# Performance work log

Measured on AMD Instinct MI355X. Metric: run time of the kernel, lower is better.

## Reference

```python
import jax, jax.numpy as jnp
import numpy as np

M, N, D = 100000, 64, 128  # points, channels, voxel grid side


def setup_inputs() -> dict:
    key = jax.random.key(0)
    k1, k2, k3, k4, k5 = jax.random.split(key, 5)
    rng = np.random.default_rng(0)
    # unique occupied voxels in a D^3 grid (Minkowski coords are unique)
    lin = rng.choice(D ** 3, size=M, replace=False)
    coords = np.stack(np.unravel_index(lin, (D, D, D)), axis=1).astype(np.int32)
    w_scale = 0.02  # ~1/sqrt(fan_in=27*N)
    return {
        "feats": jax.random.normal(k1, (M, N), dtype=jnp.float32),
        "W1": jax.random.normal(k2, (27, N, N), dtype=jnp.float32) * w_scale,
        "b1": jax.random.normal(k3, (N,), dtype=jnp.float32) * 0.01,
        "W2": jax.random.normal(k4, (27, N, N), dtype=jnp.float32) * w_scale,
        "b2": jax.random.normal(k5, (N,), dtype=jnp.float32) * 0.01,
        "coords": jnp.asarray(coords),
        "grid_size": D,
    }


def reference(feats, W1, b1, W2, b2, coords, grid_size):
    Dg = grid_size
    m = feats.shape[0]
    # dense hash: linear voxel id -> point index (-1 if empty)
    lin = (coords[:, 0].astype(jnp.int32) * Dg + coords[:, 1]) * Dg + coords[:, 2]
    lookup = jnp.full((Dg * Dg * Dg,), -1, dtype=jnp.int32).at[lin].set(
        jnp.arange(m, dtype=jnp.int32))
    offsets = jnp.array([[i, j, k] for i in (-1, 0, 1) for j in (-1, 0, 1)
                         for k in (-1, 0, 1)], dtype=jnp.int32)  # [27,3]

    def sparse_conv(x, W, b):
        # out[u] = b + sum_k W_k^T gather(x, u+off_k); scan over 27 offsets keeps
        # only one [M,N] gathered buffer live (memory-bound gather-GEMM-scatter)
        def step(acc, wk_off):
            W_k, off = wk_off
            nc = coords + off  # [M,3]
            inb = jnp.all((nc >= 0) & (nc < Dg), axis=1)
            nlin = (nc[:, 0] * Dg + nc[:, 1]) * Dg + nc[:, 2]
            nidx = lookup[jnp.where(inb, nlin, 0)]
            valid = inb & (nidx >= 0)
            g = jnp.where(valid[:, None], x[jnp.maximum(nidx, 0)], 0.0)  # [M,N]
            return acc + g @ W_k, None
        init = jnp.zeros_like(x) + b
        out, _ = jax.lax.scan(step, init, (W, offsets))
        return out

    h = jax.nn.relu(sparse_conv(feats, W1, b1))
    return jax.nn.relu(sparse_conv(h, W2, b2))
```

## Files before the change

kernel.cpp:

```cpp
#include <hip/hip_runtime.h>
#include <hip/hip_bf16.h>
#include <cstdint>
#include <cstddef>

typedef _Float16 half8 __attribute__((ext_vector_type(8)));
typedef float floatx16 __attribute__((ext_vector_type(16)));

#define DGRID 128
#define D3 (DGRID * DGRID * DGRID)
#define WSZ (2 * 27 * 4096)

__global__ void prep(const int* __restrict__ coords, const float* __restrict__ feats,
                     const float* __restrict__ W1, const float* __restrict__ W2,
                     int* __restrict__ lookup, _Float16* __restrict__ Whf,
                     _Float16* __restrict__ h0, _Float16* __restrict__ h, int M) {
    int tid = blockIdx.x * 256 + threadIdx.x;
    if (tid < WSZ) {
        int idx = tid;
        int j = idx & 7;
        int l = (idx >> 3) & 63;
        int f = (idx >> 9) & 7;
        int kL = idx >> 12;
        int k = kL % 27, L = kL / 27;
        int kk = f & 3, ct = f >> 2;
        int c = kk * 16 + (l >> 5) * 8 + j;
        int n = ct * 32 + (l & 31);
        const float* W = L ? W2 : W1;
        Whf[idx] = (_Float16)W[k * 4096 + c * 64 + n];
        return;
    }
    tid -= WSZ;
    if (tid < M) {
        int x = coords[3 * tid], y = coords[3 * tid + 1], z = coords[3 * tid + 2];
        lookup[(x * DGRID + y) * DGRID + z] = tid;
        return;
    }
    tid -= M;
    if (tid < 64) {
        h0[(size_t)M * 64 + tid] = (_Float16)0.f;
        h[(size_t)M * 64 + tid] = (_Float16)0.f;
        return;
    }
    tid -= 64;
    if (tid < M * 8) {
        const float4* src = (const float4*)feats + (size_t)tid * 2;
        float4 f0 = src[0], f1 = src[1];
        half8 v;
        v[0] = (_Float16)f0.x; v[1] = (_Float16)f0.y;
        v[2] = (_Float16)f0.z; v[3] = (_Float16)f0.w;
        v[4] = (_Float16)f1.x; v[5] = (_Float16)f1.y;
        v[6] = (_Float16)f1.z; v[7] = (_Float16)f1.w;
        ((half8*)h0)[tid] = v;
    }
}

__global__ void build_nbr(const int* __restrict__ coords, const int* __restrict__ lookup,
                          int* __restrict__ nbr, int M) {
    int m = blockIdx.x * 256 + threadIdx.x;
    if (m >= M) return;
    int x = coords[3 * m], y = coords[3 * m + 1], z = coords[3 * m + 2];
#pragma unroll
    for (int k = 0; k < 27; ++k) {
        int nx = x + k / 9 - 1, ny = y + (k / 3) % 3 - 1, nz = z + k % 3 - 1;
        int nidx = M;
        if (((unsigned)nx < DGRID) && ((unsigned)ny < DGRID) && ((unsigned)nz < DGRID)) {
            int v = lookup[(nx * DGRID + ny) * DGRID + nz];
            if ((unsigned)v < (unsigned)M) nidx = v;
        }
        nbr[(size_t)k * M + m] = nidx;
    }
}

template <bool OUT_F16>
__global__ __launch_bounds__(64, 2) void spconv(const _Float16* __restrict__ x,
                                                const _Float16* __restrict__ Whf,
                                                const float* __restrict__ bias,
                                                const int* __restrict__ nbr,
                                                void* __restrict__ outp, int M) {
    const int lane = threadIdx.x;
    const int lrow = lane & 31;
    const int lhalf = lane >> 5;
    const int mw = blockIdx.x * 64;
    const int gm0 = mw + lrow;
    const int gm1 = mw + 32 + lrow;
    const int gmc0 = gm0 < M ? gm0 : M - 1;
    const int gmc1 = gm1 < M ? gm1 : M - 1;

    floatx16 acc[4];
#pragma unroll
    for (int i = 0; i < 4; ++i)
#pragma unroll
        for (int j = 0; j < 16; ++j) acc[i][j] = 0.0f;

    const half8* wb = (const half8*)Whf + lane;

    auto loadB = [&](half8* dst, int k) {
#pragma unroll
        for (int f = 0; f < 8; ++f) dst[f] = wb[(k * 8 + f) * 64];
    };
    auto loadA = [&](half8* dst, int n0, int n1) {
        const half8* p0 = (const half8*)(x + (size_t)n0 * 64 + lhalf * 8);
        const half8* p1 = (const half8*)(x + (size_t)n1 * 64 + lhalf * 8);
#pragma unroll
        for (int kk = 0; kk < 4; ++kk) {
            dst[kk] = p0[kk * 2];
            dst[4 + kk] = p1[kk * 2];
        }
    };

    int nv0[4], nv1[4];
#pragma unroll
    for (int j = 0; j < 3; ++j) {
        nv0[j] = nbr[(size_t)j * M + gmc0];
        nv1[j] = nbr[(size_t)j * M + gmc1];
    }

    half8 Ar[3][8], Br[2][8];
    loadB(Br[0], 0);
    loadA(Ar[0], nv0[0], nv1[0]);
    loadA(Ar[1], nv0[1], nv1[1]);

#pragma unroll
    for (int i = 0; i < 27; ++i) {
        {
            int jn = i + 3;
            if (jn < 27) {
                nv0[jn & 3] = nbr[(size_t)jn * M + gmc0];
                nv1[jn & 3] = nbr[(size_t)jn * M + gmc1];
            }
        }
        if (i + 1 < 27) loadB(Br[(i + 1) & 1], i + 1);
        {
            int ja = i + 2;
            if (ja < 27) loadA(Ar[ja % 3], nv0[ja & 3], nv1[ja & 3]);
        }
        __builtin_amdgcn_sched_barrier(0);
        half8* A = Ar[i % 3];
        half8* B = Br[i & 1];
#pragma unroll
        for (int kk = 0; kk < 4; ++kk)
#pragma unroll
            for (int rt = 0; rt < 2; ++rt)
#pragma unroll
                for (int ct = 0; ct < 2; ++ct)
                    acc[rt * 2 + ct] = __builtin_amdgcn_mfma_f32_32x32x16_f16(
                        A[rt * 4 + kk], B[ct * 4 + kk], acc[rt * 2 + ct], 0, 0, 0);
    }

    const float bv0 = bias[lrow], bv1 = bias[32 + lrow];
#pragma unroll
    for (int rt = 0; rt < 2; ++rt)
#pragma unroll
        for (int ct = 0; ct < 2; ++ct) {
            const float bb = ct ? bv1 : bv0;
#pragma unroll
            for (int reg = 0; reg < 16; ++reg) {
                int row = (reg & 3) + 8 * (reg >> 2) + 4 * lhalf;
                int g = mw + rt * 32 + row;
                if (g < M) {
                    float v = acc[rt * 2 + ct][reg] + bb;
                    v = v > 0.f ? v : 0.f;
                    size_t off = (size_t)g * 64 + ct * 32 + lrow;
                    if constexpr (OUT_F16)
                        ((_Float16*)outp)[off] = (_Float16)v;
                    else
                        ((float*)outp)[off] = v;
                }
            }
        }
}

extern "C" void kernel_launch(void* const* d_in, const int* in_sizes, int n_in,
                              void* d_out, int out_size, void* d_ws, size_t ws_size,
                              hipStream_t stream) {
    const float* feats = (const float*)d_in[0];
    const float* W1 = (const float*)d_in[1];
    const float* b1 = (const float*)d_in[2];
    const float* W2 = (const float*)d_in[3];
    const float* b2 = (const float*)d_in[4];
    const int* coords = (const int*)d_in[5];
    const int M = in_sizes[0] / 64;

    int* lookup = (int*)d_ws;
    int* nbr = lookup + (size_t)D3;
    _Float16* h = (_Float16*)(nbr + (size_t)27 * M);
    _Float16* h0 = h + (size_t)(M + 1) * 64;
    _Float16* Whf = h0 + (size_t)(M + 1) * 64;
    size_t need = (size_t)D3 * 4 + (size_t)27 * M * 4 +
                  2 * (size_t)(M + 1) * 64 * 2 + (size_t)WSZ * 2;
    if (ws_size < need) return;

    long long pt = (long long)WSZ + M + 64 + (long long)M * 8;
    prep<<<(int)((pt + 255) / 256), 256, 0, stream>>>(coords, feats, W1, W2, lookup, Whf,
                                                      h0, h, M);
    build_nbr<<<(M + 255) / 256, 256, 0, stream>>>(coords, lookup, nbr, M);

    int cb = (M + 63) / 64;
    spconv<true><<<cb, 64, 0, stream>>>(h0, Whf, b1, nbr, (void*)h, M);
    spconv<false><<<cb, 64, 0, stream>>>(h, Whf + (size_t)27 * 4096, b2, nbr, d_out, M);
}
```

Before: 186.6 us.

## Fuse prep, neighbor build and both convolutions into one cooperative kernel

Replaces the four separate launches with a single cooperative persistent kernel that uses grid-wide syncs between prep, neighbor-table build and the two conv layers. Work is distributed with grid-stride loops, and each 256-thread block runs four waves, each looping over 64-row tiles. This removes launch gaps but caps the grid at 512 blocks and binds the conv to persistent scheduling with launch bounds of 256 threads. That can cut occupancy or latency hiding compared with one small block per tile. A fallback multi-kernel path remains if the cooperative launch fails.

```diff
diff --git a/kernel.cpp b/kernel.cpp
--- a/kernel.cpp
+++ b/kernel.cpp
@@ -1,7 +1,10 @@
 #include <hip/hip_runtime.h>
 #include <hip/hip_bf16.h>
+#include <hip/hip_cooperative_groups.h>
 #include <cstdint>
 #include <cstddef>
+
+namespace cg = cooperative_groups;
 
 typedef _Float16 half8 __attribute__((ext_vector_type(8)));
 typedef float floatx16 __attribute__((ext_vector_type(16)));
@@ -10,13 +13,15 @@
 #define D3 (DGRID * DGRID * DGRID)
 #define WSZ (2 * 27 * 4096)
 
-__global__ void prep(const int* __restrict__ coords, const float* __restrict__ feats,
-                     const float* __restrict__ W1, const float* __restrict__ W2,
-                     int* __restrict__ lookup, _Float16* __restrict__ Whf,
-                     _Float16* __restrict__ h0, _Float16* __restrict__ h, int M) {
-    int tid = blockIdx.x * 256 + threadIdx.x;
-    if (tid < WSZ) {
-        int idx = tid;
+__device__ __forceinline__ void do_prep(int tid, int NT, const int* __restrict__ coords,
+                                        const float* __restrict__ feats,
+                                        const float* __restrict__ W1,
+                                        const float* __restrict__ W2,
+                                        int* __restrict__ lookup,
+                                        _Float16* __restrict__ Whf,
+                                        _Float16* __restrict__ h0,
+                                        _Float16* __restrict__ h, int M) {
+    for (int idx = tid; idx < WSZ; idx += NT) {
         int j = idx & 7;
         int l = (idx >> 3) & 63;
         int f = (idx >> 9) & 7;
@@ -27,60 +32,55 @@
         int n = ct * 32 + (l & 31);
         const float* W = L ? W2 : W1;
         Whf[idx] = (_Float16)W[k * 4096 + c * 64 + n];
-        return;
-    }
-    tid -= WSZ;
-    if (tid < M) {
-        int x = coords[3 * tid], y = coords[3 * tid + 1], z = coords[3 * tid + 2];
-        lookup[(x * DGRID + y) * DGRID + z] = tid;
-        return;
-    }
-    tid -= M;
-    if (tid < 64) {
-        h0[(size_t)M * 64 + tid] = (_Float16)0.f;
-        h[(size_t)M * 64 + tid] = (_Float16)0.f;
-        return;
-    }
-    tid -= 64;
-    if (tid < M * 8) {
-        const float4* src = (const float4*)feats + (size_t)tid * 2;
+    }
+    for (int i = tid; i < M * 8; i += NT) {
+        const float4* src = (const float4*)feats + (size_t)i * 2;
         float4 f0 = src[0], f1 = src[1];
         half8 v;
         v[0] = (_Float16)f0.x; v[1] = (_Float16)f0.y;
         v[2] = (_Float16)f0.z; v[3] = (_Float16)f0.w;
         v[4] = (_Float16)f1.x; v[5] = (_Float16)f1.y;
         v[6] = (_Float16)f1.z; v[7] = (_Float16)f1.w;
-        ((half8*)h0)[tid] = v;
-    }
-}
-
-__global__ void build_nbr(const int* __restrict__ coords, const int* __restrict__ lookup,
-                          int* __restrict__ nbr, int M) {
-    int m = blockIdx.x * 256 + threadIdx.x;
-    if (m >= M) return;
-    int x = coords[3 * m], y = coords[3 * m + 1], z = coords[3 * m + 2];
-#pragma unroll
-    for (int k = 0; k < 27; ++k) {
-        int nx = x + k / 9 - 1, ny = y + (k / 3) % 3 - 1, nz = z + k % 3 - 1;
-        int nidx = M;
-        if (((unsigned)nx < DGRID) && ((unsigned)ny < DGRID) && ((unsigned)nz < DGRID)) {
-            int v = lookup[(nx * DGRID + ny) * DGRID + nz];
-            if ((unsigned)v < (unsigned)M) nidx = v;
-        }
-        nbr[(size_t)k * M + m] = nidx;
+        ((half8*)h0)[i] = v;
+    }
+    for (int m = tid; m < M; m += NT) {
+        int x = coords[3 * m], y = coords[3 * m + 1], z = coords[3 * m + 2];
+        lookup[(x * DGRID + y) * DGRID + z] = m;
+    }
+    if (tid < 64) {
+        h0[(size_t)M * 64 + tid] = (_Float16)0.f;
+        h[(size_t)M * 64 + tid] = (_Float16)0.f;
+    }
+}
+
+__device__ __forceinline__ void do_nbr(int tid, int NT, const int* __restrict__ coords,
+                                       const int* __restrict__ lookup,
+                                       int* __restrict__ nbr, int M) {
+    for (int m = tid; m < M; m += NT) {
+        int x = coords[3 * m], y = coords[3 * m + 1], z = coords[3 * m + 2];
+#pragma unroll
+        for (int k = 0; k < 27; ++k) {
+            int nx = x + k / 9 - 1, ny = y + (k / 3) % 3 - 1, nz = z + k % 3 - 1;
+            int nidx = M;
+            if (((unsigned)nx < DGRID) && ((unsigned)ny < DGRID) &&
+                ((unsigned)nz < DGRID)) {
+                int v = lookup[(nx * DGRID + ny) * DGRID + nz];
+                if ((unsigned)v < (unsigned)M) nidx = v;
+            }
+            nbr[(size_t)k * M + m] = nidx;
+        }
     }
 }
 
 template <bool OUT_F16>
-__global__ __launch_bounds__(64, 2) void spconv(const _Float16* __restrict__ x,
-                                                const _Float16* __restrict__ Whf,
-                                                const float* __restrict__ bias,
-                                                const int* __restrict__ nbr,
-                                                void* __restrict__ outp, int M) {
-    const int lane = threadIdx.x;
+__device__ __forceinline__ void conv_tile(const _Float16* __restrict__ x,
+                                          const _Float16* __restrict__ Wfrag,
+                                          const float* __restrict__ bias,
+                                          const int* __restrict__ nbr,
+                                          void* __restrict__ outp, int M, int lane,
+                                          int mw) {
     const int lrow = lane & 31;
     const int lhalf = lane >> 5;
-    const int mw = blockIdx.x * 64;
     const int gm0 = mw + lrow;
     const int gm1 = mw + 32 + lrow;
     const int gmc0 = gm0 < M ? gm0 : M - 1;
@@ -92,7 +92,7 @@
 #pragma unroll
         for (int j = 0; j < 16; ++j) acc[i][j] = 0.0f;
 
-    const half8* wb = (const half8*)Whf + lane;
+    const half8* wb = (const half8*)Wfrag + lane;
 
     auto loadB = [&](half8* dst, int k) {
 #pragma unroll
@@ -170,6 +170,59 @@
         }
 }
 
+__global__ __launch_bounds__(256, 2) void fused(const int* __restrict__ coords,
+                                                const float* __restrict__ feats,
+                                                const float* __restrict__ W1,
+                                                const float* __restrict__ b1,
+                                                const float* __restrict__ W2,
+                                                const float* __restrict__ b2,
+                                                int* __restrict__ lookup,
+                                                _Float16* __restrict__ Whf,
+                                                _Float16* __restrict__ h0,
+                                                _Float16* __restrict__ h,
+                                                int* __restrict__ nbr,
+                                                float* __restrict__ out, int M) {
+    cg::grid_group grid = cg::this_grid();
+    const int tid = blockIdx.x * 256 + threadIdx.x;
+    const int NT = gridDim.x * 256;
+
+    do_prep(tid, NT, coords, feats, W1, W2, lookup, Whf, h0, h, M);
+    grid.sync();
+    do_nbr(tid, NT, coords, lookup, nbr, M);
+    grid.sync();
+
+    const int lane = threadIdx.x & 63;
+    const int wave = blockIdx.x * 4 + (threadIdx.x >> 6);
+    const int NW = gridDim.x * 4;
+    const int NTILES = (M + 63) / 64;
+
+    for (int t = wave; t < NTILES; t += NW)
+        conv_tile<true>(h0, Whf, b1, nbr, (void*)h, M, lane, t * 64);
+    grid.sync();
+    for (int t = wave; t < NTILES; t += NW)
+        conv_tile<false>(h, Whf + (size_t)27 * 4096, b2, nbr, (void*)out, M, lane, t * 64);
+}
+
+__global__ __launch_bounds__(256) void prep_k(const int* coords, const float* feats,
+                                              const float* W1, const float* W2,
+                                              int* lookup, _Float16* Whf, _Float16* h0,
+                                              _Float16* h, int M) {
+    do_prep(blockIdx.x * 256 + threadIdx.x, gridDim.x * 256, coords, feats, W1, W2,
+            lookup, Whf, h0, h, M);
+}
+__global__ __launch_bounds__(256) void nbr_k(const int* coords, const int* lookup,
+                                             int* nbr, int M) {
+    do_nbr(blockIdx.x * 256 + threadIdx.x, gridDim.x * 256, coords, lookup, nbr, M);
+}
+template <bool OUT_F16>
+__global__ __launch_bounds__(64, 2) void conv_k(const _Float16* __restrict__ x,
+                                                const _Float16* __restrict__ Whf,
+                                                const float* __restrict__ bias,
+                                                const int* __restrict__ nbr,
+                                                void* __restrict__ outp, int M) {
+    conv_tile<OUT_F16>(x, Whf, bias, nbr, outp, M, (int)threadIdx.x, blockIdx.x * 64);
+}
+
 extern "C" void kernel_launch(void* const* d_in, const int* in_sizes, int n_in,
                               void* d_out, int out_size, void* d_ws, size_t ws_size,
                               hipStream_t stream) {
@@ -190,12 +243,25 @@
                   2 * (size_t)(M + 1) * 64 * 2 + (size_t)WSZ * 2;
     if (ws_size < need) return;
 
-    long long pt = (long long)WSZ + M + 64 + (long long)M * 8;
-    prep<<<(int)((pt + 255) / 256), 256, 0, stream>>>(coords, feats, W1, W2, lookup, Whf,
-                                                      h0, h, M);
-    build_nbr<<<(M + 255) / 256, 256, 0, stream>>>(coords, lookup, nbr, M);
-
-    int cb = (M + 63) / 64;
-    spconv<true><<<cb, 64, 0, stream>>>(h0, Whf, b1, nbr, (void*)h, M);
-    spconv<false><<<cb, 64, 0, stream>>>(h, Whf + (size_t)27 * 4096, b2, nbr, d_out, M);
-}
+    const int NTILES = (M + 63) / 64;
+    int coopGrid = (NTILES + 3) / 4;
+    if (coopGrid > 512) coopGrid = 512;
+    float* out = (float*)d_out;
+
+    int Mv = M;
+    void* args[] = {(void*)&coords, (void*)&feats, (void*)&W1,  (void*)&b1,
+                    (void*)&W2,     (void*)&b2,    (void*)&lookup, (void*)&Whf,
+                    (void*)&h0,     (void*)&h,     (void*)&nbr,  (void*)&out,
+                    (void*)&Mv};
+    hipError_t e = hipLaunchCooperativeKernel((const void*)fused, dim3(coopGrid),
+                                              dim3(256), args, 0, stream);
+    if (e != hipSuccess) {
+        long long pw = (long long)WSZ + (long long)M * 8;
+        prep_k<<<(int)((pw + 255) / 256), 256, 0, stream>>>(coords, feats, W1, W2, lookup,
+                                                            Whf, h0, h, M);
+        nbr_k<<<(M + 255) / 256, 256, 0, stream>>>(coords, lookup, nbr, M);
+        conv_k<true><<<NTILES, 64, 0, stream>>>(h0, Whf, b1, nbr, (void*)h, M);
+        conv_k<false><<<NTILES, 64, 0, stream>>>(h, Whf + (size_t)27 * 4096, b2, nbr,
+                                                 d_out, M);
+    }
+}
```

Result: slower. 515.9 us (+176.5%).

## Halve spconv rows per wave and batch z-neighbor lookups in build_nbr

Applied to the files above, without the earlier changes.

The sparse conv kernel now processes 32 output rows per 64-lane block instead of 64, which halves accumulator and A-register usage and doubles the block count. The occupancy hint is raised from 2 to 3. Separately, build_nbr loads three consecutive z entries of the lookup table in one 12-byte read per (dx,dy) pair instead of 27 scalar loads. The trade-off is that each weight tile is now reused over fewer rows, so weight reads from cache double per output row.

```diff
diff --git a/kernel.cpp b/kernel.cpp
--- a/kernel.cpp
+++ b/kernel.cpp
@@ -9,6 +9,8 @@
 #define DGRID 128
 #define D3 (DGRID * DGRID * DGRID)
 #define WSZ (2 * 27 * 4096)
+
+struct __attribute__((aligned(4))) I3 { int a, b, c; };
 
 __global__ void prep(const int* __restrict__ coords, const float* __restrict__ feats,
                      const float* __restrict__ W1, const float* __restrict__ W2,
@@ -59,20 +61,35 @@
     int m = blockIdx.x * 256 + threadIdx.x;
     if (m >= M) return;
     int x = coords[3 * m], y = coords[3 * m + 1], z = coords[3 * m + 2];
-#pragma unroll
-    for (int k = 0; k < 27; ++k) {
-        int nx = x + k / 9 - 1, ny = y + (k / 3) % 3 - 1, nz = z + k % 3 - 1;
-        int nidx = M;
-        if (((unsigned)nx < DGRID) && ((unsigned)ny < DGRID) && ((unsigned)nz < DGRID)) {
-            int v = lookup[(nx * DGRID + ny) * DGRID + nz];
-            if ((unsigned)v < (unsigned)M) nidx = v;
-        }
-        nbr[(size_t)k * M + m] = nidx;
+    int zlo = z - 1;
+    if (zlo < 0) zlo = 0;
+    if (zlo > DGRID - 3) zlo = DGRID - 3;
+    const int zi = z - zlo;
+#pragma unroll
+    for (int dx = -1; dx <= 1; ++dx) {
+#pragma unroll
+        for (int dy = -1; dy <= 1; ++dy) {
+            int nx = x + dx, ny = y + dy;
+            int v0 = -1, v1 = -1, v2 = -1;
+            if (((unsigned)nx < DGRID) && ((unsigned)ny < DGRID)) {
+                I3 t = *(const I3*)(lookup + ((nx * DGRID + ny) * DGRID + zlo));
+                v0 = t.a; v1 = t.b; v2 = t.c;
+            }
+#pragma unroll
+            for (int dz = -1; dz <= 1; ++dz) {
+                int zc = z + dz;
+                int i = zi + dz;
+                int val = (i == 0) ? v0 : (i == 1) ? v1 : v2;
+                int nidx = M;
+                if (((unsigned)zc < DGRID) && ((unsigned)val < (unsigned)M)) nidx = val;
+                nbr[(size_t)((dx + 1) * 9 + (dy + 1) * 3 + (dz + 1)) * M + m] = nidx;
+            }
+        }
     }
 }
 
 template <bool OUT_F16>
-__global__ __launch_bounds__(64, 2) void spconv(const _Float16* __restrict__ x,
+__global__ __launch_bounds__(64, 3) void spconv(const _Float16* __restrict__ x,
                                                 const _Float16* __restrict__ Whf,
                                                 const float* __restrict__ bias,
                                                 const int* __restrict__ nbr,
@@ -80,15 +97,13 @@
     const int lane = threadIdx.x;
     const int lrow = lane & 31;
     const int lhalf = lane >> 5;
-    const int mw = blockIdx.x * 64;
-    const int gm0 = mw + lrow;
-    const int gm1 = mw + 32 + lrow;
-    const int gmc0 = gm0 < M ? gm0 : M - 1;
-    const int gmc1 = gm1 < M ? gm1 : M - 1;
-
-    floatx16 acc[4];
-#pragma unroll
-    for (int i = 0; i < 4; ++i)
+    const int mw = blockIdx.x * 32;
+    const int gm = mw + lrow;
+    const int gmc = gm < M ? gm : M - 1;
+
+    floatx16 acc[2];
+#pragma unroll
+    for (int i = 0; i < 2; ++i)
 #pragma unroll
         for (int j = 0; j < 16; ++j) acc[i][j] = 0.0f;
 
@@ -98,41 +113,31 @@
 #pragma unroll
         for (int f = 0; f < 8; ++f) dst[f] = wb[(k * 8 + f) * 64];
     };
-    auto loadA = [&](half8* dst, int n0, int n1) {
-        const half8* p0 = (const half8*)(x + (size_t)n0 * 64 + lhalf * 8);
-        const half8* p1 = (const half8*)(x + (size_t)n1 * 64 + lhalf * 8);
-#pragma unroll
-        for (int kk = 0; kk < 4; ++kk) {
-            dst[kk] = p0[kk * 2];
-            dst[4 + kk] = p1[kk * 2];
-        }
+    auto loadA = [&](half8* dst, int n) {
+        const half8* p = (const half8*)(x + (size_t)n * 64 + lhalf * 8);
+#pragma unroll
+        for (int kk = 0; kk < 4; ++kk) dst[kk] = p[kk * 2];
     };
 
-    int nv0[4], nv1[4];
-#pragma unroll
-    for (int j = 0; j < 3; ++j) {
-        nv0[j] = nbr[(size_t)j * M + gmc0];
-        nv1[j] = nbr[(size_t)j * M + gmc1];
-    }
-
-    half8 Ar[3][8], Br[2][8];
+    int nv[4];
+#pragma unroll
+    for (int j = 0; j < 3; ++j) nv[j] = nbr[(size_t)j * M + gmc];
+
+    half8 Ar[3][4], Br[2][8];
     loadB(Br[0], 0);
-    loadA(Ar[0], nv0[0], nv1[0]);
-    loadA(Ar[1], nv0[1], nv1[1]);
+    loadA(Ar[0], nv[0]);
+    loadA(Ar[1], nv[1]);
 
 #pragma unroll
     for (int i = 0; i < 27; ++i) {
         {
             int jn = i + 3;
-            if (jn < 27) {
-                nv0[jn & 3] = nbr[(size_t)jn * M + gmc0];
-                nv1[jn & 3] = nbr[(size_t)jn * M + gmc1];
-            }
+            if (jn < 27) nv[jn & 3] = nbr[(size_t)jn * M + gmc];
         }
         if (i + 1 < 27) loadB(Br[(i + 1) & 1], i + 1);
         {
             int ja = i + 2;
-            if (ja < 27) loadA(Ar[ja % 3], nv0[ja & 3], nv1[ja & 3]);
+            if (ja < 27) loadA(Ar[ja % 3], nv[ja & 3]);
         }
         __builtin_amdgcn_sched_barrier(0);
         half8* A = Ar[i % 3];
@@ -140,34 +145,30 @@
 #pragma unroll
         for (int kk = 0; kk < 4; ++kk)
 #pragma unroll
-            for (int rt = 0; rt < 2; ++rt)
-#pragma unroll
-                for (int ct = 0; ct < 2; ++ct)
-                    acc[rt * 2 + ct] = __builtin_amdgcn_mfma_f32_32x32x16_f16(
-                        A[rt * 4 + kk], B[ct * 4 + kk], acc[rt * 2 + ct], 0, 0, 0);
+            for (int ct = 0; ct < 2; ++ct)
+                acc[ct] = __builtin_amdgcn_mfma_f32_32x32x16_f16(A[kk], B[ct * 4 + kk],
+                                                                 acc[ct], 0, 0, 0);
     }
 
     const float bv0 = bias[lrow], bv1 = bias[32 + lrow];
 #pragma unroll
-    for (int rt = 0; rt < 2; ++rt)
-#pragma unroll
-        for (int ct = 0; ct < 2; ++ct) {
-            const float bb = ct ? bv1 : bv0;
-#pragma unroll
-            for (int reg = 0; reg < 16; ++reg) {
-                int row = (reg & 3) + 8 * (reg >> 2) + 4 * lhalf;
-                int g = mw + rt * 32 + row;
-                if (g < M) {
-                    float v = acc[rt * 2 + ct][reg] + bb;
-                    v = v > 0.f ? v : 0.f;
-                    size_t off = (size_t)g * 64 + ct * 32 + lrow;
-                    if constexpr (OUT_F16)
-                        ((_Float16*)outp)[off] = (_Float16)v;
-                    else
-                        ((float*)outp)[off] = v;
-                }
+    for (int ct = 0; ct < 2; ++ct) {
+        const float bb = ct ? bv1 : bv0;
+#pragma unroll
+        for (int reg = 0; reg < 16; ++reg) {
+            int row = (reg & 3) + 8 * (reg >> 2) + 4 * lhalf;
+            int g = mw + row;
+            if (g < M) {
+                float v = acc[ct][reg] + bb;
+                v = v > 0.f ? v : 0.f;
+                size_t off = (size_t)g * 64 + ct * 32 + lrow;
+                if constexpr (OUT_F16)
+                    ((_Float16*)outp)[off] = (_Float16)v;
+                else
+                    ((float*)outp)[off] = v;
             }
         }
+    }
 }
 
 extern "C" void kernel_launch(void* const* d_in, const int* in_sizes, int n_in,
@@ -195,7 +196,7 @@
                                                       h0, h, M);
     build_nbr<<<(M + 255) / 256, 256, 0, stream>>>(coords, lookup, nbr, M);
 
-    int cb = (M + 63) / 64;
+    int cb = (M + 31) / 32;
     spconv<true><<<cb, 64, 0, stream>>>(h0, Whf, b1, nbr, (void*)h, M);
     spconv<false><<<cb, 64, 0, stream>>>(h, Whf + (size_t)27 * 4096, b2, nbr, d_out, M);
 }
```

Result: slower. 194.1 us (+4.0%).

## Fuse neighbor-table build into first sparse conv and stage indices in LDS

Applied to the files above, without the earlier changes.

Removes the separate build_nbr kernel. The first conv now computes the 27 neighbor indices itself, reading three consecutive z entries of the lookup per (dx,dy) pair with a single 12-byte load, and writes them to global memory for the second conv. Both convs stage the per-block neighbor indices in shared memory, so the main loop reads them from LDS instead of global. This saves one launch and some lookup traffic, at the cost of a serialized prologue before the MFMA loop and extra LDS use that may reduce occupancy.

```diff
diff --git a/kernel.cpp b/kernel.cpp
--- a/kernel.cpp
+++ b/kernel.cpp
@@ -9,6 +9,8 @@
 #define DGRID 128
 #define D3 (DGRID * DGRID * DGRID)
 #define WSZ (2 * 27 * 4096)
+
+struct __attribute__((aligned(4))) I3 { int a, b, c; };
 
 __global__ void prep(const int* __restrict__ coords, const float* __restrict__ feats,
                      const float* __restrict__ W1, const float* __restrict__ W2,
@@ -54,37 +56,63 @@
     }
 }
 
-__global__ void build_nbr(const int* __restrict__ coords, const int* __restrict__ lookup,
-                          int* __restrict__ nbr, int M) {
-    int m = blockIdx.x * 256 + threadIdx.x;
-    if (m >= M) return;
-    int x = coords[3 * m], y = coords[3 * m + 1], z = coords[3 * m + 2];
-#pragma unroll
-    for (int k = 0; k < 27; ++k) {
-        int nx = x + k / 9 - 1, ny = y + (k / 3) % 3 - 1, nz = z + k % 3 - 1;
-        int nidx = M;
-        if (((unsigned)nx < DGRID) && ((unsigned)ny < DGRID) && ((unsigned)nz < DGRID)) {
-            int v = lookup[(nx * DGRID + ny) * DGRID + nz];
-            if ((unsigned)v < (unsigned)M) nidx = v;
-        }
-        nbr[(size_t)k * M + m] = nidx;
-    }
-}
-
-template <bool OUT_F16>
+template <bool FIRST, bool OUT_F16>
 __global__ __launch_bounds__(64, 2) void spconv(const _Float16* __restrict__ x,
                                                 const _Float16* __restrict__ Whf,
                                                 const float* __restrict__ bias,
-                                                const int* __restrict__ nbr,
+                                                const int* __restrict__ coords,
+                                                const int* __restrict__ lookup,
+                                                int* __restrict__ nbr,
                                                 void* __restrict__ outp, int M) {
+    __shared__ int nvs[27 * 64];
     const int lane = threadIdx.x;
     const int lrow = lane & 31;
     const int lhalf = lane >> 5;
     const int mw = blockIdx.x * 64;
-    const int gm0 = mw + lrow;
-    const int gm1 = mw + 32 + lrow;
-    const int gmc0 = gm0 < M ? gm0 : M - 1;
-    const int gmc1 = gm1 < M ? gm1 : M - 1;
+
+    {
+        const int row = mw + lane;
+        if constexpr (FIRST) {
+            if (row < M) {
+                int X = coords[3 * row], Y = coords[3 * row + 1], Z = coords[3 * row + 2];
+                int zlo = Z - 1;
+                if (zlo < 0) zlo = 0;
+                if (zlo > DGRID - 3) zlo = DGRID - 3;
+                const int zi = Z - zlo;
+#pragma unroll
+                for (int dx = -1; dx <= 1; ++dx)
+#pragma unroll
+                    for (int dy = -1; dy <= 1; ++dy) {
+                        int nx = X + dx, ny = Y + dy;
+                        int v0 = -1, v1 = -1, v2 = -1;
+                        if (((unsigned)nx < DGRID) && ((unsigned)ny < DGRID)) {
+                            I3 t = *(const I3*)(lookup + ((nx * DGRID + ny) * DGRID + zlo));
+                            v0 = t.a; v1 = t.b; v2 = t.c;
+                        }
+#pragma unroll
+                        for (int dz = -1; dz <= 1; ++dz) {
+                            int zc = Z + dz;
+                            int i = zi + dz;
+                            int val = (i == 0) ? v0 : (i == 1) ? v1 : v2;
+                            int nidx = M;
+                            if (((unsigned)zc < DGRID) && ((unsigned)val < (unsigned)M))
+                                nidx = val;
+                            int k = (dx + 1) * 9 + (dy + 1) * 3 + (dz + 1);
+                            nvs[k * 64 + lane] = nidx;
+                            nbr[(size_t)k * M + row] = nidx;
+                        }
+                    }
+            } else {
+#pragma unroll
+                for (int k = 0; k < 27; ++k) nvs[k * 64 + lane] = M;
+            }
+        } else {
+            const int rc = row < M ? row : M - 1;
+#pragma unroll
+            for (int k = 0; k < 27; ++k) nvs[k * 64 + lane] = nbr[(size_t)k * M + rc];
+        }
+    }
+    __syncthreads();
 
     floatx16 acc[4];
 #pragma unroll
@@ -111,8 +139,8 @@
     int nv0[4], nv1[4];
 #pragma unroll
     for (int j = 0; j < 3; ++j) {
-        nv0[j] = nbr[(size_t)j * M + gmc0];
-        nv1[j] = nbr[(size_t)j * M + gmc1];
+        nv0[j] = nvs[j * 64 + lrow];
+        nv1[j] = nvs[j * 64 + 32 + lrow];
     }
 
     half8 Ar[3][8], Br[2][8];
@@ -125,8 +153,8 @@
         {
             int jn = i + 3;
             if (jn < 27) {
-                nv0[jn & 3] = nbr[(size_t)jn * M + gmc0];
-                nv1[jn & 3] = nbr[(size_t)jn * M + gmc1];
+                nv0[jn & 3] = nvs[jn * 64 + lrow];
+                nv1[jn & 3] = nvs[jn * 64 + 32 + lrow];
             }
         }
         if (i + 1 < 27) loadB(Br[(i + 1) & 1], i + 1);
@@ -193,9 +221,10 @@
     long long pt = (long long)WSZ + M + 64 + (long long)M * 8;
     prep<<<(int)((pt + 255) / 256), 256, 0, stream>>>(coords, feats, W1, W2, lookup, Whf,
                                                       h0, h, M);
-    build_nbr<<<(M + 255) / 256, 256, 0, stream>>>(coords, lookup, nbr, M);
 
     int cb = (M + 63) / 64;
-    spconv<true><<<cb, 64, 0, stream>>>(h0, Whf, b1, nbr, (void*)h, M);
-    spconv<false><<<cb, 64, 0, stream>>>(h, Whf + (size_t)27 * 4096, b2, nbr, d_out, M);
+    spconv<true, true><<<cb, 64, 0, stream>>>(h0, Whf, b1, coords, lookup, nbr,
+                                              (void*)h, M);
+    spconv<false, false><<<cb, 64, 0, stream>>>(h, Whf + (size_t)27 * 4096, b2, coords,
+                                                lookup, nbr, d_out, M);
 }
```

After: 170.3 us. 1.1x faster.
